# Performance work log

Hardware: AMD Instinct MI355X
Metric: run time of the kernel (lower is better)

Reference implementation:

```python
import jax, jax.numpy as jnp
import numpy as np

MARGIN = 1.0
N, D = 4096, 512
NUM_CLASSES = 64


def setup_inputs() -> dict:
    key = jax.random.key(0)
    k1, k2 = jax.random.split(key)
    inputs = jax.random.normal(k1, (N, D), dtype=jnp.float32)
    targets = jax.random.randint(k2, (N,), 0, NUM_CLASSES, dtype=jnp.int64)
    return {"inputs": inputs, "targets": targets}


def reference(inputs, targets):
    n = inputs.shape[0]
    sq = jnp.sum(inputs * inputs, axis=1)  # [n]
    # squared Euclidean distances, clamped at 0 (matches relu in original)
    d2 = jnp.maximum(sq[:, None] + sq[None, :] - 2.0 * (inputs @ inputs.T), 0.0)
    # safe sqrt (zero entries get 0, matching forward; avoids NaN grads)
    dist = jnp.where(d2 > 0, jnp.sqrt(jnp.where(d2 > 0, d2, 1.0)), 0.0)  # [n,n]

    same = targets[:, None] == targets[None, :]
    eye = jnp.eye(n, dtype=bool)
    pos_mask = same & ~eye          # positives, diagonal excluded
    neg_mask = ~same                # negatives (diagonal is same-label, excluded)

    # per-row sum_k exp(margin - d_ik) over negatives  (replaces per-pair loop)
    neg_sum = jnp.sum(jnp.where(neg_mask, jnp.exp(MARGIN - dist), 0.0), axis=1)  # [n]

    # J_ij = log(neg_sum_i + neg_sum_j) + d_ij for positive pairs
    J = jnp.log(neg_sum[:, None] + neg_sum[None, :]) + dist
    triu_pos = jnp.triu(pos_mask)   # loop iterated over upper-triangular positives
    hinge2 = jnp.where(triu_pos, jax.nn.relu(J) ** 2, 0.0)

    # original divides by count of ALL positive entries (both triangles)
    len_p = jnp.sum(pos_mask).astype(jnp.float32)
    return jnp.sum(hinge2) / len_p
```

## Files before the change

kernel.cpp:

```cpp
#include <hip/hip_runtime.h>
#include <math.h>

#define NN 4096
#define DD 512
#define MARGINF 1.0f
#define NCLS 64
#define MAXM 160
#define TRI (MAXM * (MAXM - 1) / 2)
#define NBLK 2080

typedef __attribute__((ext_vector_type(8))) short bf16x8;
typedef __attribute__((ext_vector_type(4))) float f32x4;

#define WS_SQ   0
#define WS_NS   4096
#define WS_LOSS 8192
#define WS_CNT  8256
#define WS_RK   8320
#define WS_MEM  12416
#define WS_XB   32768
#define WS_PD   1081344

__device__ __forceinline__ unsigned short f2bf(float f) {
    unsigned u = __float_as_uint(f);
    u += 0x7fffu + ((u >> 16) & 1u);
    return (unsigned short)(u >> 16);
}

__device__ __forceinline__ void gl_lds16(const void* g, void* l) {
    __builtin_amdgcn_global_load_lds(
        (__attribute__((address_space(1))) unsigned int*)g,
        (__attribute__((address_space(3))) unsigned int*)l,
        16, 0, 0);
}

__global__ __launch_bounds__(256) void prep_kernel(const float* __restrict__ X,
                                                   float* __restrict__ ws) {
    const int wv = threadIdx.x >> 6, lane = threadIdx.x & 63;
    const int row = blockIdx.x * 4 + wv;
    const float4* xr = (const float4*)(X + (size_t)row * DD);
    float4 a = xr[lane], b = xr[lane + 64];
    float s = a.x * a.x + a.y * a.y + a.z * a.z + a.w * a.w
            + b.x * b.x + b.y * b.y + b.z * b.z + b.w * b.w;
#pragma unroll
    for (int off = 32; off; off >>= 1) s += __shfl_down(s, off, 64);
    if (lane == 0) { ws[WS_SQ + row] = s; ws[WS_NS + row] = 0.0f; }
    ushort4 pa = {f2bf(a.x), f2bf(a.y), f2bf(a.z), f2bf(a.w)};
    ushort4 pb = {f2bf(b.x), f2bf(b.y), f2bf(b.z), f2bf(b.w)};
    ushort4* xb = (ushort4*)((unsigned short*)(ws + WS_XB) + (size_t)row * DD);
    xb[lane] = pa;
    xb[lane + 64] = pb;
    if (blockIdx.x == 0) {
        if (threadIdx.x < NCLS) ((int*)(ws + WS_CNT))[threadIdx.x] = 0;
        if (threadIdx.x == 0) ws[WS_LOSS] = 0.0f;
    }
}

__global__ __launch_bounds__(256) void class_build_kernel(const int* __restrict__ tgt,
                                                          float* __restrict__ ws) {
    const int t = blockIdx.x * 256 + threadIdx.x;
    const int c = tgt[t];
    int p = atomicAdd(&((int*)(ws + WS_CNT))[c], 1);
    ((int*)(ws + WS_RK))[t] = p;
    if (p < MAXM) ((int*)(ws + WS_MEM))[c * MAXM + p] = t;
}

__global__ __launch_bounds__(256, 8) void negsum_kernel(const int* __restrict__ tgt,
                                                        float* __restrict__ ws) {
    __shared__ unsigned short As[64 * 32];
    __shared__ unsigned short Bs[64 * 32];

    const int bidx = blockIdx.x;
    int bj = (int)((sqrtf(8.0f * (float)bidx + 1.0f) - 1.0f) * 0.5f);
    while (bj * (bj + 1) / 2 > bidx) --bj;
    while ((bj + 1) * (bj + 2) / 2 <= bidx) ++bj;
    const int bi = bidx - bj * (bj + 1) / 2;
    const int i0 = bi * 64, j0 = bj * 64;

    const int tid = threadIdx.x;
    const int w = tid >> 6, lane = tid & 63;
    const unsigned short* Xb = (const unsigned short*)(ws + WS_XB);

    const int srow = w * 16 + (lane >> 2);
    const int sc = (((lane & 3) - (lane >> 3)) & 3) * 8;
    const unsigned short* gA = Xb + (size_t)(i0 + srow) * DD + sc;
    const unsigned short* gB = Xb + (size_t)(j0 + srow) * DD + sc;
    unsigned short* lA = As + w * 512;
    unsigned short* lB = Bs + w * 512;

    const int m_ = lane & 15, q = lane >> 4;
    const int wr = (w & 1) * 32, wc = (w >> 1) * 32;
    const int sl = ((q + (m_ >> 1)) & 3) * 8;

    f32x4 acc[2][2] = {};

    for (int it = 0; it < 16; ++it) {
        __syncthreads();
        gl_lds16(gA + it * 32, lA);
        gl_lds16(gB + it * 32, lB);
        __syncthreads();
        bf16x8 af[2], bfr[2];
#pragma unroll
        for (int u = 0; u < 2; ++u)
            af[u] = *(const bf16x8*)(As + (wr + u * 16 + m_) * 32 + sl);
#pragma unroll
        for (int v = 0; v < 2; ++v)
            bfr[v] = *(const bf16x8*)(Bs + (wc + v * 16 + m_) * 32 + sl);
#pragma unroll
        for (int u = 0; u < 2; ++u)
#pragma unroll
            for (int v = 0; v < 2; ++v)
                acc[u][v] = __builtin_amdgcn_mfma_f32_16x16x32_bf16(
                    af[u], bfr[v], acc[u][v], 0, 0, 0);
    }

    const float* sq = ws + WS_SQ;
    float* ns = ws + WS_NS;
    const int* rk = (const int*)(ws + WS_RK);
    float* posd = ws + WS_PD;
    float sjv[2]; int tjv[2], jv[2];
#pragma unroll
    for (int v = 0; v < 2; ++v) {
        int j = j0 + wc + v * 16 + m_;
        jv[v] = j;
        sjv[v] = sq[j];
        tjv[v] = tgt[j];
    }
    float colp[2] = {0.0f, 0.0f};
#pragma unroll
    for (int u = 0; u < 2; ++u) {
#pragma unroll
        for (int r = 0; r < 4; ++r) {
            const int i = i0 + wr + u * 16 + q * 4 + r;
            const float si = sq[i];
            const int ti = tgt[i];
            float rp = 0.0f;
#pragma unroll
            for (int v = 0; v < 2; ++v) {
                float d2 = si + sjv[v] - 2.0f * acc[u][v][r];
                float dist = d2 > 0.0f ? sqrtf(d2) : 0.0f;
                if (tjv[v] != ti) {
                    float e = __expf(MARGINF - dist);
                    rp += e;
                    colp[v] += e;
                } else if (i < jv[v]) {
                    int ra = rk[i], rb = rk[jv[v]];
                    if (ra < MAXM && rb < MAXM) {
                        int hi = ra > rb ? ra : rb;
                        int lo = ra > rb ? rb : ra;
                        posd[ti * TRI + hi * (hi - 1) / 2 + lo] = dist;
                    }
                }
            }
            rp += __shfl_xor(rp, 1, 64);
            rp += __shfl_xor(rp, 2, 64);
            rp += __shfl_xor(rp, 4, 64);
            rp += __shfl_xor(rp, 8, 64);
            if (m_ == 0) atomicAdd(&ns[i], rp);
        }
    }
    if (bi != bj) {
#pragma unroll
        for (int v = 0; v < 2; ++v) {
            float cp = colp[v];
            cp += __shfl_xor(cp, 16, 64);
            cp += __shfl_xor(cp, 32, 64);
            if (q == 0) atomicAdd(&ns[jv[v]], cp);
        }
    }
}

__global__ __launch_bounds__(256) void pair2_kernel(float* __restrict__ ws) {
    __shared__ float wsum[4];
    const int c = blockIdx.x;
    int mc = ((const int*)(ws + WS_CNT))[c];
    if (mc > MAXM) mc = MAXM;
    const int P = mc * (mc - 1) / 2;
    const int* mem = (const int*)(ws + WS_MEM) + c * MAXM;
    const float* pd = ws + WS_PD + c * TRI;
    const float* ns = ws + WS_NS;
    float lsum = 0.0f;
    for (int p = threadIdx.x; p < P; p += 256) {
        int b = (int)((1.0f + sqrtf(1.0f + 8.0f * (float)p)) * 0.5f);
        while (b * (b - 1) / 2 > p) --b;
        while ((b + 1) * b / 2 <= p) ++b;
        const int a = p - b * (b - 1) / 2;
        const float dist = pd[b * (b - 1) / 2 + a];
        const int i = mem[a], j = mem[b];
        float J = __logf(ns[i] + ns[j]) + dist;
        float h = fmaxf(J, 0.0f);
        lsum += h * h;
    }
#pragma unroll
    for (int off = 32; off; off >>= 1) lsum += __shfl_xor(lsum, off, 64);
    const int wv = threadIdx.x >> 6, lane = threadIdx.x & 63;
    if (lane == 0) wsum[wv] = lsum;
    __syncthreads();
    if (threadIdx.x == 0) {
        float s = wsum[0] + wsum[1] + wsum[2] + wsum[3];
        if (s != 0.0f) atomicAdd(&ws[WS_LOSS], s);
    }
}

__global__ void finalize_kernel(const float* __restrict__ ws, float* __restrict__ out) {
    const int t = threadIdx.x;
    int mcv = (t < NCLS) ? ((const int*)(ws + WS_CNT))[t] : 0;
    float lp = (float)(mcv * (mcv - 1));
#pragma unroll
    for (int off = 32; off; off >>= 1) lp += __shfl_down(lp, off, 64);
    if (t == 0) out[0] = ws[WS_LOSS] / lp;
}

extern "C" void kernel_launch(void* const* d_in, const int* in_sizes, int n_in,
                              void* d_out, int out_size, void* d_ws, size_t ws_size,
                              hipStream_t stream) {
    const float* X  = (const float*)d_in[0];
    const int*  tgt = (const int*)d_in[1];
    float* ws  = (float*)d_ws;
    float* out = (float*)d_out;

    hipLaunchKernelGGL(prep_kernel, dim3(NN / 4), dim3(256), 0, stream, X, ws);
    hipLaunchKernelGGL(class_build_kernel, dim3(NN / 256), dim3(256), 0, stream, tgt, ws);
    hipLaunchKernelGGL(negsum_kernel, dim3(NBLK), dim3(256), 0, stream, tgt, ws);
    hipLaunchKernelGGL(pair2_kernel, dim3(NCLS), dim3(256), 0, stream, ws);
    hipLaunchKernelGGL(finalize_kernel, dim3(1), dim3(64), 0, stream, ws, out);
}
```

Baseline: 119.7 us.

## Load MFMA operands directly from global memory with register prefetch, dropping LDS

The negsum GEMM loop no longer stages bf16 tiles through shared memory with global_load_lds and two barriers per k-step. Each wave now loads its own A/B fragments straight from global memory into registers, prefetching the next k-step while the current MFMAs run, and the loop is fully unrolled. This removes LDS traffic and synchronisation but drops cross-wave data sharing: each operand row is fetched by two waves, which relies on L1/L2 to absorb the duplicate loads. Launch bounds are relaxed from 8 to 4 blocks per CU to allow more registers.

```diff
diff --git a/kernel.cpp b/kernel.cpp
--- a/kernel.cpp
+++ b/kernel.cpp
@@ -25,13 +25,6 @@
     unsigned u = __float_as_uint(f);
     u += 0x7fffu + ((u >> 16) & 1u);
     return (unsigned short)(u >> 16);
-}
-
-__device__ __forceinline__ void gl_lds16(const void* g, void* l) {
-    __builtin_amdgcn_global_load_lds(
-        (__attribute__((address_space(1))) unsigned int*)g,
-        (__attribute__((address_space(3))) unsigned int*)l,
-        16, 0, 0);
 }
 
 __global__ __launch_bounds__(256) void prep_kernel(const float* __restrict__ X,
@@ -65,11 +58,8 @@
     if (p < MAXM) ((int*)(ws + WS_MEM))[c * MAXM + p] = t;
 }
 
-__global__ __launch_bounds__(256, 8) void negsum_kernel(const int* __restrict__ tgt,
+__global__ __launch_bounds__(256, 4) void negsum_kernel(const int* __restrict__ tgt,
                                                         float* __restrict__ ws) {
-    __shared__ unsigned short As[64 * 32];
-    __shared__ unsigned short Bs[64 * 32];
-
     const int bidx = blockIdx.x;
     int bj = (int)((sqrtf(8.0f * (float)bidx + 1.0f) - 1.0f) * 0.5f);
     while (bj * (bj + 1) / 2 > bidx) --bj;
@@ -79,39 +69,36 @@
 
     const int tid = threadIdx.x;
     const int w = tid >> 6, lane = tid & 63;
-    const unsigned short* Xb = (const unsigned short*)(ws + WS_XB);
-
-    const int srow = w * 16 + (lane >> 2);
-    const int sc = (((lane & 3) - (lane >> 3)) & 3) * 8;
-    const unsigned short* gA = Xb + (size_t)(i0 + srow) * DD + sc;
-    const unsigned short* gB = Xb + (size_t)(j0 + srow) * DD + sc;
-    unsigned short* lA = As + w * 512;
-    unsigned short* lB = Bs + w * 512;
-
     const int m_ = lane & 15, q = lane >> 4;
     const int wr = (w & 1) * 32, wc = (w >> 1) * 32;
-    const int sl = ((q + (m_ >> 1)) & 3) * 8;
+    const unsigned short* Xb = (const unsigned short*)(ws + WS_XB);
+
+    const unsigned short* pA0 = Xb + (size_t)(i0 + wr + m_) * DD + q * 8;
+    const unsigned short* pA1 = pA0 + (size_t)16 * DD;
+    const unsigned short* pB0 = Xb + (size_t)(j0 + wc + m_) * DD + q * 8;
+    const unsigned short* pB1 = pB0 + (size_t)16 * DD;
 
     f32x4 acc[2][2] = {};
 
+    bf16x8 a0 = *(const bf16x8*)(pA0);
+    bf16x8 a1 = *(const bf16x8*)(pA1);
+    bf16x8 b0 = *(const bf16x8*)(pB0);
+    bf16x8 b1 = *(const bf16x8*)(pB1);
+
+#pragma unroll
     for (int it = 0; it < 16; ++it) {
-        __syncthreads();
-        gl_lds16(gA + it * 32, lA);
-        gl_lds16(gB + it * 32, lB);
-        __syncthreads();
-        bf16x8 af[2], bfr[2];
-#pragma unroll
-        for (int u = 0; u < 2; ++u)
-            af[u] = *(const bf16x8*)(As + (wr + u * 16 + m_) * 32 + sl);
-#pragma unroll
-        for (int v = 0; v < 2; ++v)
-            bfr[v] = *(const bf16x8*)(Bs + (wc + v * 16 + m_) * 32 + sl);
-#pragma unroll
-        for (int u = 0; u < 2; ++u)
-#pragma unroll
-            for (int v = 0; v < 2; ++v)
-                acc[u][v] = __builtin_amdgcn_mfma_f32_16x16x32_bf16(
-                    af[u], bfr[v], acc[u][v], 0, 0, 0);
+        bf16x8 na0, na1, nb0, nb1;
+        if (it < 15) {
+            na0 = *(const bf16x8*)(pA0 + (it + 1) * 32);
+            na1 = *(const bf16x8*)(pA1 + (it + 1) * 32);
+            nb0 = *(const bf16x8*)(pB0 + (it + 1) * 32);
+            nb1 = *(const bf16x8*)(pB1 + (it + 1) * 32);
+        }
+        acc[0][0] = __builtin_amdgcn_mfma_f32_16x16x32_bf16(a0, b0, acc[0][0], 0, 0, 0);
+        acc[0][1] = __builtin_amdgcn_mfma_f32_16x16x32_bf16(a0, b1, acc[0][1], 0, 0, 0);
+        acc[1][0] = __builtin_amdgcn_mfma_f32_16x16x32_bf16(a1, b0, acc[1][0], 0, 0, 0);
+        acc[1][1] = __builtin_amdgcn_mfma_f32_16x16x32_bf16(a1, b1, acc[1][1], 0, 0, 0);
+        a0 = na0; a1 = na1; b0 = nb0; b1 = nb1;
     }
 
     const float* sq = ws + WS_SQ;
```

Result: slower. 156.7 us (+31.0%).
